# Optimization experiments

Hardware: AMD Instinct MI355X
Metric: run time of the kernel (lower is better)

## Reference

```python
import jax, jax.numpy as jnp
import numpy as np

B, C, N, F_, HID = 512, 3, 128, 256, 128  # batch, channels, nodes(=in_dim), num_f(=seq), gru hidden


def setup_inputs() -> dict:
    key = jax.random.key(0)
    ks = jax.random.split(key, 12)
    s = 0.05
    inp = {
        "X": jax.random.normal(ks[0], (B, N, F_), jnp.float32),
        "H": jax.random.uniform(ks[1], (B, C, N, N), jnp.float32),
        "weight": jnp.full((1, 1), 10.0, jnp.float32),        # nn.init.constant_(weight, 10)
        "soft": jnp.full((C,), 1.0 / C, jnp.float32),          # nn.init.constant_(soft, 1/C)
        "w_ih_f": jax.random.normal(ks[2], (3 * HID, N), jnp.float32) * s,
        "w_hh_f": jax.random.normal(ks[3], (3 * HID, HID), jnp.float32) * s,
        "b_ih_f": jax.random.normal(ks[4], (3 * HID,), jnp.float32) * s,
        "b_hh_f": jax.random.normal(ks[5], (3 * HID,), jnp.float32) * s,
        "w_ih_b": jax.random.normal(ks[6], (3 * HID, N), jnp.float32) * s,
        "w_hh_b": jax.random.normal(ks[7], (3 * HID, HID), jnp.float32) * s,
        "b_ih_b": jax.random.normal(ks[8], (3 * HID,), jnp.float32) * s,
        "b_hh_b": jax.random.normal(ks[9], (3 * HID,), jnp.float32) * s,
        "bn_gamma": jnp.ones((F_,), jnp.float32),
        "bn_beta": jnp.zeros((F_,), jnp.float32),
    }
    return inp


def _gru_dir(xs, w_ih, w_hh, b_ih, b_hh):
    # xs: [T, B, in] -> ys: [T, B, HID]; torch GRU cell equations
    def cell(h, x):
        gi = x @ w_ih.T + b_ih
        gh = h @ w_hh.T + b_hh
        i_r, i_z, i_n = jnp.split(gi, 3, axis=-1)
        h_r, h_z, h_n = jnp.split(gh, 3, axis=-1)
        r = jax.nn.sigmoid(i_r + h_r)
        z = jax.nn.sigmoid(i_z + h_z)
        n = jnp.tanh(i_n + r * h_n)
        h_new = (1.0 - z) * n + z * h
        return h_new, h_new
    h0 = jnp.zeros((xs.shape[1], w_hh.shape[1]), xs.dtype)
    _, ys = jax.lax.scan(cell, h0, xs)
    return ys


def reference(X, H, weight, soft, w_ih_f, w_hh_f, b_ih_f, b_hh_f,
              w_ih_b, w_hh_b, b_ih_b, b_hh_b, bn_gamma, bn_beta):
    n = X.shape[1]
    I = jnp.eye(n, dtype=X.dtype)
    # norm(): zero the diagonal, add identity, symmetric D^-1/2 H D^-1/2 (all C channels at once)
    Hn = H * (1.0 - I) + I                              # [B,C,N,N]
    deg = jnp.sum(Hn, axis=-1)                          # [B,C,N]
    dinv = deg ** -0.5
    Hn = dinv[..., :, None] * Hn * dinv[..., None, :]
    # gcn_conv across all features/channels in one einsum; weight is a 1x1 scalar
    HX = jnp.einsum('bcnm,bmf->bcnf', Hn, X) * weight[0, 0]
    Xc = jnp.sum(jax.nn.leaky_relu(HX, 0.01) * soft[None, :, None, None], axis=1)  # [B,N,F]
    # per1 -> [B, F, N]; GRU batch_first with seq_len=F, input=N
    xs = Xc.transpose(2, 0, 1)                          # [T=F, B, N]
    yf = _gru_dir(xs, w_ih_f, w_hh_f, b_ih_f, b_hh_f)
    yb = _gru_dir(xs[::-1], w_ih_b, w_hh_b, b_ih_b, b_hh_b)[::-1]
    y = jnp.concatenate([yf, yb], axis=-1).transpose(1, 0, 2)  # [B, F, 2*HID]

    # BatchNorm1d(num_f), training-mode batch stats over (batch, length) per channel F
    mean = jnp.mean(y, axis=(0, 2), keepdims=True)
    var = jnp.var(y, axis=(0, 2), keepdims=True)
    y = bn_gamma[None, :, None] * (y - mean) / jnp.sqrt(var + 1e-5) + bn_beta[None, :, None]
    # per2 -> [B, 2*HID, F]
    return y.transpose(0, 2, 1)
```

## Files before the change

### kernel.cpp

```cpp
#include <hip/hip_runtime.h>

typedef short s8v  __attribute__((ext_vector_type(8)));
typedef float f4v  __attribute__((ext_vector_type(4)));

#define B_   512
#define C_   3
#define N_   128
#define F_   256
#define T_   256
#define HID_ 128
#define G3_  384

__device__ __forceinline__ ushort f2bf(float f) {
  union { float f; unsigned u; } v; v.f = f;
  return (ushort)((v.u + 0x7FFFu + ((v.u >> 16) & 1u)) >> 16);
}
__device__ __forceinline__ float bf2f(ushort h) {
  union { unsigned u; float f; } v; v.u = ((unsigned)h) << 16;
  return v.f;
}
__device__ __forceinline__ float rcp_(float x) { return __builtin_amdgcn_rcpf(x); }
__device__ __forceinline__ float sigm(float x) { return rcp_(1.0f + __expf(-x)); }
__device__ __forceinline__ float tanh_(float x) { return 2.0f * rcp_(1.0f + __expf(-2.0f * x)) - 1.0f; }

#define LDS_BARRIER() asm volatile("s_waitcnt lgkmcnt(0)\n\ts_barrier" ::: "memory")

__global__ void k_wcvt(const float* __restrict__ a, const float* __restrict__ b,
                       const float* __restrict__ c, const float* __restrict__ d,
                       ushort* __restrict__ o) {
  int i = blockIdx.x * 256 + threadIdx.x;
  const float* src = (i < 49152) ? a : (i < 98304) ? b : (i < 147456) ? c : d;
  o[i] = f2bf(src[i % 49152]);
}

__global__ __launch_bounds__(512) void k_hnorm(const float* __restrict__ H,
                                               ushort* __restrict__ Hn) {
  __shared__ float dvr[N_];
  const int bc = blockIdx.x;
  const int tid = threadIdx.x;
  const int r = tid >> 2;
  const int q0 = (tid & 3) * 32;
  const float* src = H + (size_t)bc * 16384 + (size_t)r * 128 + q0;

  float v[32];
  #pragma unroll
  for (int i = 0; i < 8; ++i) {
    float4 t4 = *(const float4*)&src[i * 4];
    const int c = q0 + i * 4;
    v[i * 4 + 0] = (c + 0 == r) ? 1.0f : t4.x;
    v[i * 4 + 1] = (c + 1 == r) ? 1.0f : t4.y;
    v[i * 4 + 2] = (c + 2 == r) ? 1.0f : t4.z;
    v[i * 4 + 3] = (c + 3 == r) ? 1.0f : t4.w;
  }
  float s = 0.f;
  #pragma unroll
  for (int i = 0; i < 32; ++i) s += v[i];
  s += __shfl_xor(s, 1);
  s += __shfl_xor(s, 2);
  if ((tid & 3) == 0) dvr[r] = 1.0f / sqrtf(s);
  __syncthreads();

  const float dr = dvr[r];
  ushort* dst = Hn + (size_t)bc * 16384 + (size_t)r * 128 + q0;
  #pragma unroll
  for (int i = 0; i < 8; ++i) {
    float4 dc = *(const float4*)&dvr[q0 + i * 4];
    ushort4 o;
    o.x = f2bf(v[i * 4 + 0] * dr * dc.x);
    o.y = f2bf(v[i * 4 + 1] * dr * dc.y);
    o.z = f2bf(v[i * 4 + 2] * dr * dc.z);
    o.w = f2bf(v[i * 4 + 3] * dr * dc.w);
    *(ushort4*)&dst[i * 4] = o;
  }
}

__global__ __launch_bounds__(256, 2) void k_conv2(
    const float* __restrict__ X, const ushort* __restrict__ Hn,
    const float* __restrict__ wscal, const float* __restrict__ soft,
    ushort* __restrict__ XcT) {
  __shared__ ushort hc[N_][136];
  __shared__ ushort xt[N_][136];
  const int b = blockIdx.x;
  const int tid = threadIdx.x;
  const int lane = tid & 63, w = tid >> 6;
  const int rq = lane >> 4, l15 = lane & 15;
  const float wmul = wscal[0];
  const float scf[3] = {soft[0], soft[1], soft[2]};
  const ushort* Hb = Hn + (size_t)b * C_ * N_ * N_;
  const int srow = tid >> 1;
  const int scol = (tid & 1) * 64;

  for (int fh = 0; fh < 2; ++fh) {
    __syncthreads();
    {
      const int fl4 = (tid & 31) * 4;
      const int mof = tid >> 5;
      #pragma unroll
      for (int p = 0; p < 16; ++p) {
        int m = p * 8 + mof;
        float4 v = *(const float4*)&X[((size_t)b * N_ + m) * F_ + fh * 128 + fl4];
        xt[fl4 + 0][m] = f2bf(v.x);
        xt[fl4 + 1][m] = f2bf(v.y);
        xt[fl4 + 2][m] = f2bf(v.z);
        xt[fl4 + 3][m] = f2bf(v.w);
      }
    }
    __syncthreads();

    s8v af[2][4];
    #pragma unroll
    for (int rt = 0; rt < 2; ++rt)
      #pragma unroll
      for (int kk = 0; kk < 4; ++kk)
        af[rt][kk] = *(const s8v*)&xt[w * 32 + rt * 16 + l15][kk * 32 + rq * 8];

    f4v xc[2][8];
    #pragma unroll
    for (int rt = 0; rt < 2; ++rt)
      #pragma unroll
      for (int nt = 0; nt < 8; ++nt)
        xc[rt][nt] = (f4v){0.f, 0.f, 0.f, 0.f};

    for (int c = 0; c < C_; ++c) {
      __syncthreads();
      {
        const ushort* hsrc = &Hb[((size_t)c * N_ + srow) * N_ + scol];
        #pragma unroll
        for (int p = 0; p < 8; ++p)
          *(s8v*)&hc[srow][scol + p * 8] = *(const s8v*)&hsrc[p * 8];
      }
      __syncthreads();

      f4v hx[2][8];
      #pragma unroll
      for (int rt = 0; rt < 2; ++rt)
        #pragma unroll
        for (int nt = 0; nt < 8; ++nt)
          hx[rt][nt] = (f4v){0.f, 0.f, 0.f, 0.f};
      #pragma unroll
      for (int kk = 0; kk < 4; ++kk) {
        #pragma unroll
        for (int nt = 0; nt < 8; ++nt) {
          s8v bf = *(const s8v*)&hc[nt * 16 + l15][kk * 32 + rq * 8];
          hx[0][nt] = __builtin_amdgcn_mfma_f32_16x16x32_bf16(af[0][kk], bf, hx[0][nt], 0, 0, 0);
          hx[1][nt] = __builtin_amdgcn_mfma_f32_16x16x32_bf16(af[1][kk], bf, hx[1][nt], 0, 0, 0);
        }
      }
      const float s = scf[c];
      #pragma unroll
      for (int nt = 0; nt < 8; ++nt) {
        #pragma unroll
        for (int i = 0; i < 4; ++i) {
          float v0 = hx[0][nt][i] * wmul;
          xc[0][nt][i] += s * fmaxf(v0, 0.01f * v0);
          float v1 = hx[1][nt][i] * wmul;
          xc[1][nt][i] += s * fmaxf(v1, 0.01f * v1);
        }
      }
    }
    __syncthreads();
    #pragma unroll
    for (int rt = 0; rt < 2; ++rt)
      #pragma unroll
      for (int nt = 0; nt < 8; ++nt)
        #pragma unroll
        for (int i = 0; i < 4; ++i)
          xt[w * 32 + rt * 16 + rq * 4 + i][nt * 16 + l15] = f2bf(xc[rt][nt][i]);
    __syncthreads();
    #pragma unroll
    for (int p = 0; p < 4; ++p) {
      int tl = p * 32 + (tid >> 3);
      int n0 = (tid & 7) * 16;
      size_t rowb = ((size_t)b * F_ + fh * 128 + tl) * N_;
      *(s8v*)&XcT[rowb + n0]     = *(const s8v*)&xt[tl][n0];
      *(s8v*)&XcT[rowb + n0 + 8] = *(const s8v*)&xt[tl][n0 + 8];
    }
  }
}

__global__ __launch_bounds__(512, 2) void k_gru(
    const ushort* __restrict__ XcT, const ushort* __restrict__ wbf,
    const float* __restrict__ bihf, const float* __restrict__ bhhf,
    const float* __restrict__ bihb, const float* __restrict__ bhhb,
    ushort* __restrict__ y) {
  __shared__ ushort hlds[2][16][136];
  __shared__ ushort xbuf[2][16][136];
  const int dir = blockIdx.x >> 5;
  const int chunk = blockIdx.x & 31;
  const int tid = threadIdx.x;
  const int lane = tid & 63, w = tid >> 6;
  const int rq = lane >> 4, l15 = lane & 15;
  const int jb = w * 16;
  const int jr = jb + rq * 4;
  const ushort* wih = wbf + (size_t)(dir * 2) * G3_ * HID_;
  const ushort* whh = wih + G3_ * HID_;
  const float* bih = dir ? bihb : bihf;
  const float* bhh = dir ? bhhb : bhhf;

  s8v fir[4], fiz[4], fin[4], fhr[4], fhz[4], fhn[4];
  #pragma unroll
  for (int kk = 0; kk < 4; ++kk) {
    const int ko = kk * 32 + rq * 8;
    const int row = jb + l15;
    fir[kk] = *(const s8v*)&wih[(size_t)(row)       * HID_ + ko];
    fiz[kk] = *(const s8v*)&wih[(size_t)(128 + row) * HID_ + ko];
    fin[kk] = *(const s8v*)&wih[(size_t)(256 + row) * HID_ + ko];
    fhr[kk] = *(const s8v*)&whh[(size_t)(row)       * HID_ + ko];
    fhz[kk] = *(const s8v*)&whh[(size_t)(128 + row) * HID_ + ko];
    fhn[kk] = *(const s8v*)&whh[(size_t)(256 + row) * HID_ + ko];
  }
  float4 bi_r = *(const float4*)&bih[jr],        bh_r = *(const float4*)&bhh[jr];
  float4 bi_z = *(const float4*)&bih[128 + jr],  bh_z = *(const float4*)&bhh[128 + jr];
  float4 bin4 = *(const float4*)&bih[256 + jr];
  float4 bhn4 = *(const float4*)&bhh[256 + jr];
  f4v br = {bi_r.x + bh_r.x, bi_r.y + bh_r.y, bi_r.z + bh_r.z, bi_r.w + bh_r.w};
  f4v bz = {bi_z.x + bh_z.x, bi_z.y + bh_z.y, bi_z.z + bh_z.z, bi_z.w + bh_z.w};
  f4v bin = {bin4.x, bin4.y, bin4.z, bin4.w};
  f4v bhn = {bhn4.x, bhn4.y, bhn4.z, bhn4.w};

  for (int i = tid; i < 16 * 136; i += 512) ((ushort*)hlds[0])[i] = 0;

  const int rr = tid >> 5;
  const int nq = (tid & 31) * 4;
  const size_t xrow = (size_t)(chunk * 16 + rr) * T_;
  {
    int t0 = dir ? (T_ - 1) : 0;
    *(ushort4*)&xbuf[0][rr][nq] = *(const ushort4*)&XcT[(xrow + t0) * N_ + nq];
  }
  f4v hreg = {0.f, 0.f, 0.f, 0.f};
  __syncthreads();

  for (int s = 0; s < T_; ++s) {
    const int cur = s & 1;
    const int t_in = dir ? (T_ - 1 - s) : s;
    const int sn = (s + 1 < T_) ? s + 1 : s;
    const int t_nx = dir ? (T_ - 1 - sn) : sn;
    ushort4 xn = *(const ushort4*)&XcT[(xrow + t_nx) * N_ + nq];

    f4v ar = br, az = bz, ain = bin, ahn = bhn;
    #pragma unroll
    for (int kk = 0; kk < 4; ++kk) {
      const int ko = kk * 32 + rq * 8;
      s8v xf = *(const s8v*)&xbuf[cur][l15][ko];
      s8v hf = *(const s8v*)&hlds[cur][l15][ko];
      ar  = __builtin_amdgcn_mfma_f32_16x16x32_bf16(fir[kk], xf, ar, 0, 0, 0);
      ar  = __builtin_amdgcn_mfma_f32_16x16x32_bf16(fhr[kk], hf, ar, 0, 0, 0);
      az  = __builtin_amdgcn_mfma_f32_16x16x32_bf16(fiz[kk], xf, az, 0, 0, 0);
      az  = __builtin_amdgcn_mfma_f32_16x16x32_bf16(fhz[kk], hf, az, 0, 0, 0);
      ain = __builtin_amdgcn_mfma_f32_16x16x32_bf16(fin[kk], xf, ain, 0, 0, 0);
      ahn = __builtin_amdgcn_mfma_f32_16x16x32_bf16(fhn[kk], hf, ahn, 0, 0, 0);
    }
    ushort hb[4];
    #pragma unroll
    for (int i = 0; i < 4; ++i) {
      float r = sigm(ar[i]);
      float z = sigm(az[i]);
      float n = tanh_(ain[i] + r * ahn[i]);
      float h = n + z * (hreg[i] - n);
      hreg[i] = h;
      hb[i] = f2bf(h);
    }
    ushort4 hv; hv.x = hb[0]; hv.y = hb[1]; hv.z = hb[2]; hv.w = hb[3];
    *(ushort4*)&y[((size_t)t_in * B_ + chunk * 16 + l15) * 256 + dir * 128 + jr] = hv;
    *(ushort4*)&hlds[cur ^ 1][l15][jr] = hv;
    *(ushort4*)&xbuf[cur ^ 1][rr][nq] = xn;
    LDS_BARRIER();
  }
}

__global__ void k_stats(const ushort* __restrict__ y, const float* __restrict__ gamma,
                        const float* __restrict__ beta, float* __restrict__ stats) {
  const int t = blockIdx.x, tid = threadIdx.x;
  const ushort* p = y + (size_t)t * 256 * B_;
  float s = 0.f, q = 0.f;
  for (int i = tid * 8; i < 256 * B_; i += 256 * 8) {
    s8v v = *(const s8v*)&p[i];
    #pragma unroll
    for (int e = 0; e < 8; ++e) {
      float f = bf2f((ushort)v[e]);
      s += f; q += f * f;
    }
  }
  #pragma unroll
  for (int o = 32; o; o >>= 1) { s += __shfl_xor(s, o); q += __shfl_xor(q, o); }
  __shared__ float rs[4], rq2[4];
  if ((tid & 63) == 0) { rs[tid >> 6] = s; rq2[tid >> 6] = q; }
  __syncthreads();
  if (tid == 0) {
    s = rs[0] + rs[1] + rs[2] + rs[3];
    q = rq2[0] + rq2[1] + rq2[2] + rq2[3];
    const float inv = 1.0f / (256.f * 512.f);
    float mean = s * inv;
    float var = q * inv - mean * mean;
    float istd = 1.0f / sqrtf(var + 1e-5f);
    float a = gamma[t] * istd;
    stats[2 * t] = a;
    stats[2 * t + 1] = beta[t] - mean * a;
  }
}

__global__ __launch_bounds__(256) void k_apply(
    const ushort* __restrict__ y, const float* __restrict__ stats,
    float* __restrict__ out) {
  __shared__ ushort tile[64][258];
  __shared__ float sA[64], sB[64];
  const int b = blockIdx.x;
  const int t0 = blockIdx.y * 64;
  const int tid = threadIdx.x;
  if (tid < 64) {
    sA[tid] = stats[2 * (t0 + tid)];
    sB[tid] = stats[2 * (t0 + tid) + 1];
  }
  {
    const int jc = (tid & 31) * 8;
    #pragma unroll
    for (int p = 0; p < 8; ++p) {
      int tl = p * 8 + (tid >> 5);
      *(s8v*)&tile[tl][jc] = *(const s8v*)&y[((size_t)(t0 + tl) * B_ + b) * 256 + jc];
    }
  }
  __syncthreads();
  const int tq = tid & 15;
  const int jo = tid >> 4;
  #pragma unroll
  for (int jb = 0; jb < 256; jb += 16) {
    const int j = jb + jo;
    float4 o;
    o.x = bf2f(tile[tq * 4 + 0][j]) * sA[tq * 4 + 0] + sB[tq * 4 + 0];
    o.y = bf2f(tile[tq * 4 + 1][j]) * sA[tq * 4 + 1] + sB[tq * 4 + 1];
    o.z = bf2f(tile[tq * 4 + 2][j]) * sA[tq * 4 + 2] + sB[tq * 4 + 2];
    o.w = bf2f(tile[tq * 4 + 3][j]) * sA[tq * 4 + 3] + sB[tq * 4 + 3];
    *(float4*)&out[((size_t)b * 256 + j) * 256 + t0 + tq * 4] = o;
  }
}

extern "C" void kernel_launch(void* const* d_in, const int* in_sizes, int n_in,
                              void* d_out, int out_size, void* d_ws, size_t ws_size,
                              hipStream_t stream) {
  const float* X      = (const float*)d_in[0];
  const float* H      = (const float*)d_in[1];
  const float* weight = (const float*)d_in[2];
  const float* soft   = (const float*)d_in[3];
  const float* w_ih_f = (const float*)d_in[4];
  const float* w_hh_f = (const float*)d_in[5];
  const float* b_ih_f = (const float*)d_in[6];
  const float* b_hh_f = (const float*)d_in[7];
  const float* w_ih_b = (const float*)d_in[8];
  const float* w_hh_b = (const float*)d_in[9];
  const float* b_ih_b = (const float*)d_in[10];
  const float* b_hh_b = (const float*)d_in[11];
  const float* gamma  = (const float*)d_in[12];
  const float* beta   = (const float*)d_in[13];
  float* out = (float*)d_out;

  char* ws = (char*)d_ws;
  ushort* wbf   = (ushort*)(ws);
  ushort* Hnb   = (ushort*)(ws + 393216);
  ushort* XcT   = (ushort*)(ws + 50724864);
  ushort* ybuf  = (ushort*)(ws + 84279296);
  float*  stats = (float*) (ws + 151388160);

  k_wcvt<<<768, 256, 0, stream>>>(w_ih_f, w_hh_f, w_ih_b, w_hh_b, wbf);
  k_hnorm<<<B_ * C_, 512, 0, stream>>>(H, Hnb);
  k_conv2<<<B_, 256, 0, stream>>>(X, Hnb, weight, soft, XcT);
  k_gru<<<64, 512, 0, stream>>>(XcT, wbf, b_ih_f, b_hh_f, b_ih_b, b_hh_b, ybuf);
  k_stats<<<T_, 256, 0, stream>>>(ybuf, gamma, beta, stats);
  k_apply<<<dim3(512, 4), 256, 0, stream>>>(ybuf, stats, out);
}
```

Measured before the change: 360.8 us.

## Load GRU input fragments directly into registers and split input/hidden MFMA chains

Removes the LDS staging buffer for the GRU input: each lane now loads its own bf16 input fragments straight from global memory into registers, two steps ahead, using two alternating register sets across a manually unrolled pair of steps. The input-projection MFMAs are issued before the hidden-state ones into separate accumulators, so they do not depend on the previous hidden state and can overlap with the LDS read of h. This shortens the serial per-step dependency chain and removes the LDS write of x. The cost is higher register pressure, redundant global loads across waves, and extra global latency that has to be covered by the prefetch distance.

```diff
diff --git a/kernel.cpp b/kernel.cpp
--- a/kernel.cpp
+++ b/kernel.cpp
@@ -178,13 +178,57 @@
   }
 }
 
+#define GRU_STEP(SS, CUR, XF)                                                             \
+  {                                                                                       \
+    const int s = (SS);                                                                   \
+    const int t_in = dir ? (T_ - 1 - s) : s;                                              \
+    s8v hf[4];                                                                            \
+    _Pragma("unroll")                                                                     \
+    for (int kk = 0; kk < 4; ++kk)                                                        \
+      hf[kk] = *(const s8v*)&hlds[CUR][l15][kk * 32 + rq * 8];                            \
+    f4v arx = br, azx = bz, anx = bin;                                                    \
+    _Pragma("unroll")                                                                     \
+    for (int kk = 0; kk < 4; ++kk) {                                                      \
+      arx = __builtin_amdgcn_mfma_f32_16x16x32_bf16(fir[kk], XF[kk], arx, 0, 0, 0);       \
+      azx = __builtin_amdgcn_mfma_f32_16x16x32_bf16(fiz[kk], XF[kk], azx, 0, 0, 0);       \
+      anx = __builtin_amdgcn_mfma_f32_16x16x32_bf16(fin[kk], XF[kk], anx, 0, 0, 0);       \
+    }                                                                                     \
+    {                                                                                     \
+      const int sp = (s + 2 < T_) ? s + 2 : T_ - 1;                                       \
+      const int tp = dir ? (T_ - 1 - sp) : sp;                                            \
+      _Pragma("unroll")                                                                   \
+      for (int kk = 0; kk < 4; ++kk)                                                      \
+        XF[kk] = *(const s8v*)&XcT[(xrowL + tp) * N_ + kk * 32 + rq * 8];                 \
+    }                                                                                     \
+    f4v arh = {0.f, 0.f, 0.f, 0.f}, azh = {0.f, 0.f, 0.f, 0.f}, anh = bhn;                \
+    _Pragma("unroll")                                                                     \
+    for (int kk = 0; kk < 4; ++kk) {                                                      \
+      arh = __builtin_amdgcn_mfma_f32_16x16x32_bf16(fhr[kk], hf[kk], arh, 0, 0, 0);       \
+      azh = __builtin_amdgcn_mfma_f32_16x16x32_bf16(fhz[kk], hf[kk], azh, 0, 0, 0);       \
+      anh = __builtin_amdgcn_mfma_f32_16x16x32_bf16(fhn[kk], hf[kk], anh, 0, 0, 0);       \
+    }                                                                                     \
+    ushort hb[4];                                                                         \
+    _Pragma("unroll")                                                                     \
+    for (int i = 0; i < 4; ++i) {                                                         \
+      float r = sigm(arx[i] + arh[i]);                                                    \
+      float z = sigm(azx[i] + azh[i]);                                                    \
+      float n = tanh_(anx[i] + r * anh[i]);                                               \
+      float h = n + z * (hreg[i] - n);                                                    \
+      hreg[i] = h;                                                                        \
+      hb[i] = f2bf(h);                                                                    \
+    }                                                                                     \
+    ushort4 hv; hv.x = hb[0]; hv.y = hb[1]; hv.z = hb[2]; hv.w = hb[3];                   \
+    *(ushort4*)&y[((size_t)t_in * B_ + chunk * 16 + l15) * 256 + dir * 128 + jr] = hv;    \
+    *(ushort4*)&hlds[CUR ^ 1][l15][jr] = hv;                                              \
+    LDS_BARRIER();                                                                        \
+  }
+
 __global__ __launch_bounds__(512, 2) void k_gru(
     const ushort* __restrict__ XcT, const ushort* __restrict__ wbf,
     const float* __restrict__ bihf, const float* __restrict__ bhhf,
     const float* __restrict__ bihb, const float* __restrict__ bhhb,
     ushort* __restrict__ y) {
   __shared__ ushort hlds[2][16][136];
-  __shared__ ushort xbuf[2][16][136];
   const int dir = blockIdx.x >> 5;
   const int chunk = blockIdx.x & 31;
   const int tid = threadIdx.x;
@@ -213,58 +257,30 @@
   float4 bi_z = *(const float4*)&bih[128 + jr],  bh_z = *(const float4*)&bhh[128 + jr];
   float4 bin4 = *(const float4*)&bih[256 + jr];
   float4 bhn4 = *(const float4*)&bhh[256 + jr];
-  f4v br = {bi_r.x + bh_r.x, bi_r.y + bh_r.y, bi_r.z + bh_r.z, bi_r.w + bh_r.w};
-  f4v bz = {bi_z.x + bh_z.x, bi_z.y + bh_z.y, bi_z.z + bh_z.z, bi_z.w + bh_z.w};
-  f4v bin = {bin4.x, bin4.y, bin4.z, bin4.w};
-  f4v bhn = {bhn4.x, bhn4.y, bhn4.z, bhn4.w};
+  const f4v br  = {bi_r.x + bh_r.x, bi_r.y + bh_r.y, bi_r.z + bh_r.z, bi_r.w + bh_r.w};
+  const f4v bz  = {bi_z.x + bh_z.x, bi_z.y + bh_z.y, bi_z.z + bh_z.z, bi_z.w + bh_z.w};
+  const f4v bin = {bin4.x, bin4.y, bin4.z, bin4.w};
+  const f4v bhn = {bhn4.x, bhn4.y, bhn4.z, bhn4.w};
 
   for (int i = tid; i < 16 * 136; i += 512) ((ushort*)hlds[0])[i] = 0;
 
-  const int rr = tid >> 5;
-  const int nq = (tid & 31) * 4;
-  const size_t xrow = (size_t)(chunk * 16 + rr) * T_;
+  const size_t xrowL = (size_t)(chunk * 16 + l15) * T_;
+  s8v xf0[4], xf1[4];
   {
-    int t0 = dir ? (T_ - 1) : 0;
-    *(ushort4*)&xbuf[0][rr][nq] = *(const ushort4*)&XcT[(xrow + t0) * N_ + nq];
+    const int ta = dir ? (T_ - 1) : 0;
+    const int tb = dir ? (T_ - 2) : 1;
+    #pragma unroll
+    for (int kk = 0; kk < 4; ++kk) {
+      xf0[kk] = *(const s8v*)&XcT[(xrowL + ta) * N_ + kk * 32 + rq * 8];
+      xf1[kk] = *(const s8v*)&XcT[(xrowL + tb) * N_ + kk * 32 + rq * 8];
+    }
   }
   f4v hreg = {0.f, 0.f, 0.f, 0.f};
   __syncthreads();
 
-  for (int s = 0; s < T_; ++s) {
-    const int cur = s & 1;
-    const int t_in = dir ? (T_ - 1 - s) : s;
-    const int sn = (s + 1 < T_) ? s + 1 : s;
-    const int t_nx = dir ? (T_ - 1 - sn) : sn;
-    ushort4 xn = *(const ushort4*)&XcT[(xrow + t_nx) * N_ + nq];
-
-    f4v ar = br, az = bz, ain = bin, ahn = bhn;
-    #pragma unroll
-    for (int kk = 0; kk < 4; ++kk) {
-      const int ko = kk * 32 + rq * 8;
-      s8v xf = *(const s8v*)&xbuf[cur][l15][ko];
-      s8v hf = *(const s8v*)&hlds[cur][l15][ko];
-      ar  = __builtin_amdgcn_mfma_f32_16x16x32_bf16(fir[kk], xf, ar, 0, 0, 0);
-      ar  = __builtin_amdgcn_mfma_f32_16x16x32_bf16(fhr[kk], hf, ar, 0, 0, 0);
-      az  = __builtin_amdgcn_mfma_f32_16x16x32_bf16(fiz[kk], xf, az, 0, 0, 0);
-      az  = __builtin_amdgcn_mfma_f32_16x16x32_bf16(fhz[kk], hf, az, 0, 0, 0);
-      ain = __builtin_amdgcn_mfma_f32_16x16x32_bf16(fin[kk], xf, ain, 0, 0, 0);
-      ahn = __builtin_amdgcn_mfma_f32_16x16x32_bf16(fhn[kk], hf, ahn, 0, 0, 0);
-    }
-    ushort hb[4];
-    #pragma unroll
-    for (int i = 0; i < 4; ++i) {
-      float r = sigm(ar[i]);
-      float z = sigm(az[i]);
-      float n = tanh_(ain[i] + r * ahn[i]);
-      float h = n + z * (hreg[i] - n);
-      hreg[i] = h;
-      hb[i] = f2bf(h);
-    }
-    ushort4 hv; hv.x = hb[0]; hv.y = hb[1]; hv.z = hb[2]; hv.w = hb[3];
-    *(ushort4*)&y[((size_t)t_in * B_ + chunk * 16 + l15) * 256 + dir * 128 + jr] = hv;
-    *(ushort4*)&hlds[cur ^ 1][l15][jr] = hv;
-    *(ushort4*)&xbuf[cur ^ 1][rr][nq] = xn;
-    LDS_BARRIER();
+  for (int s2 = 0; s2 < T_ / 2; ++s2) {
+    GRU_STEP(2 * s2,     0, xf0)
+    GRU_STEP(2 * s2 + 1, 1, xf1)
   }
 }
 
```

Result: slower. 445.0 us (+23.3%).

## Split GRU gate work across specialized wave groups in 1024-thread blocks

Applied to the files above, without the earlier changes.

The GRU recurrence kernel now launches 1024 threads per block instead of 512, in two wave groups. Eight waves compute the r and z gates, convert them to bf16 and pass them through a new shared-memory buffer. The other eight waves compute the n-gate matmuls, read r and z, and finish the hidden-state update and output store. The aim is to shorten each wave's serial MFMA chain per timestep, at the cost of a second block barrier per step. It also adds bf16 rounding of the r and z gate values and lowers occupancy to one block per CU.

```diff
diff --git a/kernel.cpp b/kernel.cpp
--- a/kernel.cpp
+++ b/kernel.cpp
@@ -178,93 +178,136 @@
   }
 }
 
-__global__ __launch_bounds__(512, 2) void k_gru(
+__global__ __launch_bounds__(1024, 1) void k_gru(
     const ushort* __restrict__ XcT, const ushort* __restrict__ wbf,
     const float* __restrict__ bihf, const float* __restrict__ bhhf,
     const float* __restrict__ bihb, const float* __restrict__ bhhb,
     ushort* __restrict__ y) {
   __shared__ ushort hlds[2][16][136];
   __shared__ ushort xbuf[2][16][136];
+  __shared__ ushort rzb[16][272];
   const int dir = blockIdx.x >> 5;
   const int chunk = blockIdx.x & 31;
   const int tid = threadIdx.x;
   const int lane = tid & 63, w = tid >> 6;
   const int rq = lane >> 4, l15 = lane & 15;
-  const int jb = w * 16;
+  const bool isA = (w < 8);
+  const int jb = (isA ? w : (w - 8)) * 16;
   const int jr = jb + rq * 4;
   const ushort* wih = wbf + (size_t)(dir * 2) * G3_ * HID_;
   const ushort* whh = wih + G3_ * HID_;
   const float* bih = dir ? bihb : bihf;
   const float* bhh = dir ? bhhb : bhhf;
 
-  s8v fir[4], fiz[4], fin[4], fhr[4], fhz[4], fhn[4];
-  #pragma unroll
-  for (int kk = 0; kk < 4; ++kk) {
-    const int ko = kk * 32 + rq * 8;
-    const int row = jb + l15;
-    fir[kk] = *(const s8v*)&wih[(size_t)(row)       * HID_ + ko];
-    fiz[kk] = *(const s8v*)&wih[(size_t)(128 + row) * HID_ + ko];
-    fin[kk] = *(const s8v*)&wih[(size_t)(256 + row) * HID_ + ko];
-    fhr[kk] = *(const s8v*)&whh[(size_t)(row)       * HID_ + ko];
-    fhz[kk] = *(const s8v*)&whh[(size_t)(128 + row) * HID_ + ko];
-    fhn[kk] = *(const s8v*)&whh[(size_t)(256 + row) * HID_ + ko];
-  }
-  float4 bi_r = *(const float4*)&bih[jr],        bh_r = *(const float4*)&bhh[jr];
-  float4 bi_z = *(const float4*)&bih[128 + jr],  bh_z = *(const float4*)&bhh[128 + jr];
-  float4 bin4 = *(const float4*)&bih[256 + jr];
-  float4 bhn4 = *(const float4*)&bhh[256 + jr];
-  f4v br = {bi_r.x + bh_r.x, bi_r.y + bh_r.y, bi_r.z + bh_r.z, bi_r.w + bh_r.w};
-  f4v bz = {bi_z.x + bh_z.x, bi_z.y + bh_z.y, bi_z.z + bh_z.z, bi_z.w + bh_z.w};
-  f4v bin = {bin4.x, bin4.y, bin4.z, bin4.w};
-  f4v bhn = {bhn4.x, bhn4.y, bhn4.z, bhn4.w};
-
-  for (int i = tid; i < 16 * 136; i += 512) ((ushort*)hlds[0])[i] = 0;
-
-  const int rr = tid >> 5;
-  const int nq = (tid & 31) * 4;
-  const size_t xrow = (size_t)(chunk * 16 + rr) * T_;
-  {
-    int t0 = dir ? (T_ - 1) : 0;
-    *(ushort4*)&xbuf[0][rr][nq] = *(const ushort4*)&XcT[(xrow + t0) * N_ + nq];
-  }
-  f4v hreg = {0.f, 0.f, 0.f, 0.f};
-  __syncthreads();
-
-  for (int s = 0; s < T_; ++s) {
-    const int cur = s & 1;
-    const int t_in = dir ? (T_ - 1 - s) : s;
-    const int sn = (s + 1 < T_) ? s + 1 : s;
-    const int t_nx = dir ? (T_ - 1 - sn) : sn;
-    ushort4 xn = *(const ushort4*)&XcT[(xrow + t_nx) * N_ + nq];
-
-    f4v ar = br, az = bz, ain = bin, ahn = bhn;
+  for (int i = tid; i < 16 * 136; i += 1024) ((ushort*)hlds[0])[i] = 0;
+
+  if (isA) {
+    s8v fir[4], fiz[4], fhr[4], fhz[4];
     #pragma unroll
     for (int kk = 0; kk < 4; ++kk) {
       const int ko = kk * 32 + rq * 8;
-      s8v xf = *(const s8v*)&xbuf[cur][l15][ko];
-      s8v hf = *(const s8v*)&hlds[cur][l15][ko];
-      ar  = __builtin_amdgcn_mfma_f32_16x16x32_bf16(fir[kk], xf, ar, 0, 0, 0);
-      ar  = __builtin_amdgcn_mfma_f32_16x16x32_bf16(fhr[kk], hf, ar, 0, 0, 0);
-      az  = __builtin_amdgcn_mfma_f32_16x16x32_bf16(fiz[kk], xf, az, 0, 0, 0);
-      az  = __builtin_amdgcn_mfma_f32_16x16x32_bf16(fhz[kk], hf, az, 0, 0, 0);
-      ain = __builtin_amdgcn_mfma_f32_16x16x32_bf16(fin[kk], xf, ain, 0, 0, 0);
-      ahn = __builtin_amdgcn_mfma_f32_16x16x32_bf16(fhn[kk], hf, ahn, 0, 0, 0);
-    }
-    ushort hb[4];
-    #pragma unroll
-    for (int i = 0; i < 4; ++i) {
-      float r = sigm(ar[i]);
-      float z = sigm(az[i]);
-      float n = tanh_(ain[i] + r * ahn[i]);
-      float h = n + z * (hreg[i] - n);
-      hreg[i] = h;
-      hb[i] = f2bf(h);
-    }
-    ushort4 hv; hv.x = hb[0]; hv.y = hb[1]; hv.z = hb[2]; hv.w = hb[3];
-    *(ushort4*)&y[((size_t)t_in * B_ + chunk * 16 + l15) * 256 + dir * 128 + jr] = hv;
-    *(ushort4*)&hlds[cur ^ 1][l15][jr] = hv;
-    *(ushort4*)&xbuf[cur ^ 1][rr][nq] = xn;
-    LDS_BARRIER();
+      const int row = jb + l15;
+      fir[kk] = *(const s8v*)&wih[(size_t)(row)       * HID_ + ko];
+      fiz[kk] = *(const s8v*)&wih[(size_t)(128 + row) * HID_ + ko];
+      fhr[kk] = *(const s8v*)&whh[(size_t)(row)       * HID_ + ko];
+      fhz[kk] = *(const s8v*)&whh[(size_t)(128 + row) * HID_ + ko];
+    }
+    float4 bi_r = *(const float4*)&bih[jr],       bh_r = *(const float4*)&bhh[jr];
+    float4 bi_z = *(const float4*)&bih[128 + jr], bh_z = *(const float4*)&bhh[128 + jr];
+    const f4v br = {bi_r.x + bh_r.x, bi_r.y + bh_r.y, bi_r.z + bh_r.z, bi_r.w + bh_r.w};
+    const f4v bz = {bi_z.x + bh_z.x, bi_z.y + bh_z.y, bi_z.z + bh_z.z, bi_z.w + bh_z.w};
+
+    const int rr = tid >> 5;
+    const int nq = (tid & 31) * 4;
+    const size_t xrow = (size_t)(chunk * 16 + rr) * T_;
+    {
+      int t0 = dir ? (T_ - 1) : 0;
+      *(ushort4*)&xbuf[0][rr][nq] = *(const ushort4*)&XcT[(xrow + t0) * N_ + nq];
+    }
+    __syncthreads();
+
+    for (int s = 0; s < T_; ++s) {
+      const int cur = s & 1;
+      const int sn = (s + 1 < T_) ? s + 1 : s;
+      const int t_nx = dir ? (T_ - 1 - sn) : sn;
+      ushort4 xn = *(const ushort4*)&XcT[(xrow + t_nx) * N_ + nq];
+
+      f4v arx = br, azx = bz;
+      f4v arh = {0.f, 0.f, 0.f, 0.f}, azh = {0.f, 0.f, 0.f, 0.f};
+      #pragma unroll
+      for (int kk = 0; kk < 4; ++kk) {
+        const int ko = kk * 32 + rq * 8;
+        s8v xf = *(const s8v*)&xbuf[cur][l15][ko];
+        s8v hf = *(const s8v*)&hlds[cur][l15][ko];
+        arx = __builtin_amdgcn_mfma_f32_16x16x32_bf16(fir[kk], xf, arx, 0, 0, 0);
+        azx = __builtin_amdgcn_mfma_f32_16x16x32_bf16(fiz[kk], xf, azx, 0, 0, 0);
+        arh = __builtin_amdgcn_mfma_f32_16x16x32_bf16(fhr[kk], hf, arh, 0, 0, 0);
+        azh = __builtin_amdgcn_mfma_f32_16x16x32_bf16(fhz[kk], hf, azh, 0, 0, 0);
+      }
+      ushort4 rv, zv;
+      {
+        float r0 = sigm(arx[0] + arh[0]), r1 = sigm(arx[1] + arh[1]);
+        float r2 = sigm(arx[2] + arh[2]), r3 = sigm(arx[3] + arh[3]);
+        float z0 = sigm(azx[0] + azh[0]), z1 = sigm(azx[1] + azh[1]);
+        float z2 = sigm(azx[2] + azh[2]), z3 = sigm(azx[3] + azh[3]);
+        rv.x = f2bf(r0); rv.y = f2bf(r1); rv.z = f2bf(r2); rv.w = f2bf(r3);
+        zv.x = f2bf(z0); zv.y = f2bf(z1); zv.z = f2bf(z2); zv.w = f2bf(z3);
+      }
+      *(ushort4*)&rzb[l15][jr] = rv;
+      *(ushort4*)&rzb[l15][136 + jr] = zv;
+      LDS_BARRIER();
+      *(ushort4*)&xbuf[cur ^ 1][rr][nq] = xn;
+      LDS_BARRIER();
+    }
+  } else {
+    s8v fin[4], fhn[4];
+    #pragma unroll
+    for (int kk = 0; kk < 4; ++kk) {
+      const int ko = kk * 32 + rq * 8;
+      const int row = 256 + jb + l15;
+      fin[kk] = *(const s8v*)&wih[(size_t)row * HID_ + ko];
+      fhn[kk] = *(const s8v*)&whh[(size_t)row * HID_ + ko];
+    }
+    float4 bin4 = *(const float4*)&bih[256 + jr];
+    float4 bhn4 = *(const float4*)&bhh[256 + jr];
+    const f4v bin = {bin4.x, bin4.y, bin4.z, bin4.w};
+    const f4v bhn = {bhn4.x, bhn4.y, bhn4.z, bhn4.w};
+    f4v hreg = {0.f, 0.f, 0.f, 0.f};
+    __syncthreads();
+
+    for (int s = 0; s < T_; ++s) {
+      const int cur = s & 1;
+      const int t_in = dir ? (T_ - 1 - s) : s;
+      f4v anx = bin, anh = bhn;
+      #pragma unroll
+      for (int kk = 0; kk < 4; ++kk) {
+        const int ko = kk * 32 + rq * 8;
+        s8v xf = *(const s8v*)&xbuf[cur][l15][ko];
+        s8v hf = *(const s8v*)&hlds[cur][l15][ko];
+        anx = __builtin_amdgcn_mfma_f32_16x16x32_bf16(fin[kk], xf, anx, 0, 0, 0);
+        anh = __builtin_amdgcn_mfma_f32_16x16x32_bf16(fhn[kk], hf, anh, 0, 0, 0);
+      }
+      LDS_BARRIER();
+      ushort4 rv = *(const ushort4*)&rzb[l15][jr];
+      ushort4 zv = *(const ushort4*)&rzb[l15][136 + jr];
+      ushort hb[4];
+      {
+        float n0 = tanh_(anx[0] + bf2f(rv.x) * anh[0]);
+        float n1 = tanh_(anx[1] + bf2f(rv.y) * anh[1]);
+        float n2 = tanh_(anx[2] + bf2f(rv.z) * anh[2]);
+        float n3 = tanh_(anx[3] + bf2f(rv.w) * anh[3]);
+        float h0 = n0 + bf2f(zv.x) * (hreg[0] - n0);
+        float h1 = n1 + bf2f(zv.y) * (hreg[1] - n1);
+        float h2 = n2 + bf2f(zv.z) * (hreg[2] - n2);
+        float h3 = n3 + bf2f(zv.w) * (hreg[3] - n3);
+        hreg[0] = h0; hreg[1] = h1; hreg[2] = h2; hreg[3] = h3;
+        hb[0] = f2bf(h0); hb[1] = f2bf(h1); hb[2] = f2bf(h2); hb[3] = f2bf(h3);
+      }
+      ushort4 hv; hv.x = hb[0]; hv.y = hb[1]; hv.z = hb[2]; hv.w = hb[3];
+      *(ushort4*)&y[((size_t)t_in * B_ + chunk * 16 + l15) * 256 + dir * 128 + jr] = hv;
+      *(ushort4*)&hlds[cur ^ 1][l15][jr] = hv;
+      LDS_BARRIER();
+    }
   }
 }
 
@@ -363,7 +406,7 @@
   k_wcvt<<<768, 256, 0, stream>>>(w_ih_f, w_hh_f, w_ih_b, w_hh_b, wbf);
   k_hnorm<<<B_ * C_, 512, 0, stream>>>(H, Hnb);
   k_conv2<<<B_, 256, 0, stream>>>(X, Hnb, weight, soft, XcT);
-  k_gru<<<64, 512, 0, stream>>>(XcT, wbf, b_ih_f, b_hh_f, b_ih_b, b_hh_b, ybuf);
+  k_gru<<<64, 1024, 0, stream>>>(XcT, wbf, b_ih_f, b_hh_f, b_ih_b, b_hh_b, ybuf);
   k_stats<<<T_, 256, 0, stream>>>(ybuf, gamma, beta, stats);
   k_apply<<<dim3(512, 4), 256, 0, stream>>>(ybuf, stats, out);
 }
```

Result: slower. 457.1 us (+26.7%).

## Software-pipeline GRU input projection one step ahead of the recurrent critical path

Applied to the files above, without the earlier changes.

Splits the per-step MFMA work so the input-to-hidden projection for step s+1 is computed after the hidden state for step s is published, leaving only the three recurrent MFMAs per kk on the serial dependency chain. The x prefetch deepens to a three-step register/LDS pipeline to feed it. This shortens the latency-bound recurrence per timestep at the cost of extra live accumulator registers and a more complex buffer rotation.

```diff
diff --git a/kernel.cpp b/kernel.cpp
--- a/kernel.cpp
+++ b/kernel.cpp
@@ -213,49 +213,58 @@
   float4 bi_z = *(const float4*)&bih[128 + jr],  bh_z = *(const float4*)&bhh[128 + jr];
   float4 bin4 = *(const float4*)&bih[256 + jr];
   float4 bhn4 = *(const float4*)&bhh[256 + jr];
-  f4v br = {bi_r.x + bh_r.x, bi_r.y + bh_r.y, bi_r.z + bh_r.z, bi_r.w + bh_r.w};
-  f4v bz = {bi_z.x + bh_z.x, bi_z.y + bh_z.y, bi_z.z + bh_z.z, bi_z.w + bh_z.w};
-  f4v bin = {bin4.x, bin4.y, bin4.z, bin4.w};
-  f4v bhn = {bhn4.x, bhn4.y, bhn4.z, bhn4.w};
+  const f4v br  = {bi_r.x + bh_r.x, bi_r.y + bh_r.y, bi_r.z + bh_r.z, bi_r.w + bh_r.w};
+  const f4v bz  = {bi_z.x + bh_z.x, bi_z.y + bh_z.y, bi_z.z + bh_z.z, bi_z.w + bh_z.w};
+  const f4v bin = {bin4.x, bin4.y, bin4.z, bin4.w};
+  const f4v bhn = {bhn4.x, bhn4.y, bhn4.z, bhn4.w};
 
   for (int i = tid; i < 16 * 136; i += 512) ((ushort*)hlds[0])[i] = 0;
 
   const int rr = tid >> 5;
   const int nq = (tid & 31) * 4;
   const size_t xrow = (size_t)(chunk * 16 + rr) * T_;
+
+  ushort4 R;
   {
-    int t0 = dir ? (T_ - 1) : 0;
+    const int t0 = dir ? (T_ - 1) : 0;
+    const int t1 = dir ? (T_ - 2) : 1;
+    const int t2 = dir ? (T_ - 3) : 2;
     *(ushort4*)&xbuf[0][rr][nq] = *(const ushort4*)&XcT[(xrow + t0) * N_ + nq];
+    *(ushort4*)&xbuf[1][rr][nq] = *(const ushort4*)&XcT[(xrow + t1) * N_ + nq];
+    R = *(const ushort4*)&XcT[(xrow + t2) * N_ + nq];
   }
   f4v hreg = {0.f, 0.f, 0.f, 0.f};
+  __syncthreads();
+
+  f4v xar = br, xaz = bz, xan = bin;
+  #pragma unroll
+  for (int kk = 0; kk < 4; ++kk) {
+    const int ko = kk * 32 + rq * 8;
+    s8v xf = *(const s8v*)&xbuf[0][l15][ko];
+    xar = __builtin_amdgcn_mfma_f32_16x16x32_bf16(fir[kk], xf, xar, 0, 0, 0);
+    xaz = __builtin_amdgcn_mfma_f32_16x16x32_bf16(fiz[kk], xf, xaz, 0, 0, 0);
+    xan = __builtin_amdgcn_mfma_f32_16x16x32_bf16(fin[kk], xf, xan, 0, 0, 0);
+  }
   __syncthreads();
 
   for (int s = 0; s < T_; ++s) {
     const int cur = s & 1;
     const int t_in = dir ? (T_ - 1 - s) : s;
-    const int sn = (s + 1 < T_) ? s + 1 : s;
-    const int t_nx = dir ? (T_ - 1 - sn) : sn;
-    ushort4 xn = *(const ushort4*)&XcT[(xrow + t_nx) * N_ + nq];
-
-    f4v ar = br, az = bz, ain = bin, ahn = bhn;
+
+    f4v har = {0.f, 0.f, 0.f, 0.f}, haz = {0.f, 0.f, 0.f, 0.f}, han = bhn;
     #pragma unroll
     for (int kk = 0; kk < 4; ++kk) {
-      const int ko = kk * 32 + rq * 8;
-      s8v xf = *(const s8v*)&xbuf[cur][l15][ko];
-      s8v hf = *(const s8v*)&hlds[cur][l15][ko];
-      ar  = __builtin_amdgcn_mfma_f32_16x16x32_bf16(fir[kk], xf, ar, 0, 0, 0);
-      ar  = __builtin_amdgcn_mfma_f32_16x16x32_bf16(fhr[kk], hf, ar, 0, 0, 0);
-      az  = __builtin_amdgcn_mfma_f32_16x16x32_bf16(fiz[kk], xf, az, 0, 0, 0);
-      az  = __builtin_amdgcn_mfma_f32_16x16x32_bf16(fhz[kk], hf, az, 0, 0, 0);
-      ain = __builtin_amdgcn_mfma_f32_16x16x32_bf16(fin[kk], xf, ain, 0, 0, 0);
-      ahn = __builtin_amdgcn_mfma_f32_16x16x32_bf16(fhn[kk], hf, ahn, 0, 0, 0);
+      s8v hf = *(const s8v*)&hlds[cur][l15][kk * 32 + rq * 8];
+      har = __builtin_amdgcn_mfma_f32_16x16x32_bf16(fhr[kk], hf, har, 0, 0, 0);
+      haz = __builtin_amdgcn_mfma_f32_16x16x32_bf16(fhz[kk], hf, haz, 0, 0, 0);
+      han = __builtin_amdgcn_mfma_f32_16x16x32_bf16(fhn[kk], hf, han, 0, 0, 0);
     }
     ushort hb[4];
     #pragma unroll
     for (int i = 0; i < 4; ++i) {
-      float r = sigm(ar[i]);
-      float z = sigm(az[i]);
-      float n = tanh_(ain[i] + r * ahn[i]);
+      float r = sigm(xar[i] + har[i]);
+      float z = sigm(xaz[i] + haz[i]);
+      float n = tanh_(xan[i] + r * han[i]);
       float h = n + z * (hreg[i] - n);
       hreg[i] = h;
       hb[i] = f2bf(h);
@@ -263,7 +272,21 @@
     ushort4 hv; hv.x = hb[0]; hv.y = hb[1]; hv.z = hb[2]; hv.w = hb[3];
     *(ushort4*)&y[((size_t)t_in * B_ + chunk * 16 + l15) * 256 + dir * 128 + jr] = hv;
     *(ushort4*)&hlds[cur ^ 1][l15][jr] = hv;
-    *(ushort4*)&xbuf[cur ^ 1][rr][nq] = xn;
+
+    *(ushort4*)&xbuf[cur][rr][nq] = R;
+    {
+      const int sp = (s + 3 < T_) ? s + 3 : T_ - 1;
+      const int tp = dir ? (T_ - 1 - sp) : sp;
+      R = *(const ushort4*)&XcT[(xrow + tp) * N_ + nq];
+    }
+    xar = br; xaz = bz; xan = bin;
+    #pragma unroll
+    for (int kk = 0; kk < 4; ++kk) {
+      s8v xf = *(const s8v*)&xbuf[cur ^ 1][l15][kk * 32 + rq * 8];
+      xar = __builtin_amdgcn_mfma_f32_16x16x32_bf16(fir[kk], xf, xar, 0, 0, 0);
+      xaz = __builtin_amdgcn_mfma_f32_16x16x32_bf16(fiz[kk], xf, xaz, 0, 0, 0);
+      xan = __builtin_amdgcn_mfma_f32_16x16x32_bf16(fin[kk], xf, xan, 0, 0, 0);
+    }
     LDS_BARRIER();
   }
 }
```

Measured after the change: 391.9 us. 8.6% more time.
